# Kernel optimization log

Hardware: AMD Instinct MI355X
Metric: run time of the kernel (lower is better)

Reference implementation:

```python
import jax, jax.numpy as jnp
import numpy as np

N, E, C_IN, C_H, HOPS = 100000, 1600000, 10, 128, 3
LN_EPS = 1e-5


def setup_inputs() -> dict:
    key = jax.random.key(0)
    ks = jax.random.split(key, 8)
    s = 0.05  # weight init scale
    return {
        "x": jax.random.normal(ks[0], (N, C_IN), dtype=jnp.float32),
        "W_in": jax.random.normal(ks[1], (C_H, C_IN), dtype=jnp.float32) * s,
        "b_in": jnp.zeros((C_H,), jnp.float32),
        "hop_W": jax.random.normal(ks[2], (HOPS, C_H, C_H), dtype=jnp.float32) * s,
        "hop_b": jnp.zeros((HOPS, C_H), jnp.float32),
        "hop_g": jnp.ones((HOPS, C_H), jnp.float32),
        "hop_be": jnp.zeros((HOPS, C_H), jnp.float32),
        "gates": jax.random.normal(ks[3], (HOPS, C_H), dtype=jnp.float32),
        "fW": jax.random.normal(ks[4], (C_H, C_H), dtype=jnp.float32) * s,
        "fb": jnp.zeros((C_H,), jnp.float32),
        "fg": jnp.ones((C_H,), jnp.float32),
        "fbe": jnp.zeros((C_H,), jnp.float32),
        "edge_index": jax.random.randint(ks[5], (2, E), 0, N, dtype=jnp.int64) if jax.config.jax_enable_x64 else jax.random.randint(ks[5], (2, E), 0, N).astype(jnp.int32),
        "edge_attr": jax.random.randint(ks[6], (E,), 0, 5).astype(jnp.int32),
    }


def _layernorm(h, g, b):
    mu = h.mean(-1, keepdims=True)
    var = ((h - mu) ** 2).mean(-1, keepdims=True)  # biased var (torch LayerNorm)
    return (h - mu) * jax.lax.rsqrt(var + LN_EPS) * g + b


def _mpnn(x, src, dst, W, b, g, be):
    # ResidualMPNNLayer: scatter-max aggregate of x[src] at dst, linear, LN, residual relu.
    # dst entries equal to n act as a dummy bucket (for masked-out edges).
    n = x.shape[0]
    agg = jax.ops.segment_max(x[src], dst, num_segments=n + 1)[:n]
    # nodes with no incoming messages: torch_scatter fills with 0
    agg = jnp.where(jnp.isfinite(agg), agg, 0.0)
    return jax.nn.relu(_layernorm(agg @ W.T + b, g, be) + x)


def reference(x, W_in, b_in, hop_W, hop_b, hop_g, hop_be, gates, fW, fb, fg, fbe, edge_index, edge_attr):
    src, dst = edge_index[0], edge_index[1]
    n = x.shape[0]

    # ThreeHopSmallBlock
    h = jax.nn.relu(x @ W_in.T + b_in)  # [N, C_H]
    hop_outs = []
    for i in range(HOPS):
        h = _mpnn(h, src, dst, hop_W[i], hop_b[i], hop_g[i], hop_be[i])
        hop_outs.append(h)
    node_features = sum(o * jax.nn.sigmoid(gates[i]) for i, o in enumerate(hop_outs))
    # dropout inactive at inference

    # polygon subgraph: edges with attr == 3; masked edges scatter to dummy bucket n
    poly = edge_attr == 3
    dst_p = jnp.where(poly, dst, n)
    sub = _mpnn(node_features, src, dst_p, fW, fb, fg, fbe)  # [N, C_H]

    neg_inf = jnp.float32(-jnp.inf)
    fill = jnp.float32(1e-4)

    # sink nodes = unique destinations of polygon edges
    sink_mask = jax.ops.segment_sum(poly.astype(jnp.int32), dst, num_segments=n) > 0
    v2 = jnp.max(jnp.where(sink_mask[:, None], sub, neg_inf), axis=0, keepdims=True)
    v2 = jnp.where(jnp.any(sink_mask), v2, fill)

    # remaining nodes: NOT (x[:,0] > 0.1)
    rem = ~(x[:, 0] > 0.1)
    v3 = jnp.max(jnp.where(rem[:, None], node_features, neg_inf), axis=0, keepdims=True)
    v3 = jnp.where(jnp.any(rem), v3, fill)

    return jnp.concatenate([v2, v3], axis=0)  # [2, C_H]
```

## Files before the change

### kernel.cpp

```cpp
#include <hip/hip_runtime.h>
#include <hip/hip_bf16.h>
#include <cstdint>

#define N_NODES 100000
#define N_EDGES 1600000
#define C_IN    10
#define C_H     128
#define LN_EPS  1e-5f

#define SCAN_BLOCKS 98

typedef unsigned short u16x2 __attribute__((ext_vector_type(2)));

static __device__ inline unsigned pkmax(unsigned a, unsigned b) {
    u16x2 x = __builtin_bit_cast(u16x2, a), y = __builtin_bit_cast(u16x2, b);
    return __builtin_bit_cast(unsigned, __builtin_elementwise_max(x, y));
}
static __device__ inline unsigned bf16rne(float f) {
    unsigned u = __float_as_uint(f);
    return (u + 0x7FFFu + ((u >> 16) & 1u)) >> 16;
}
static __device__ inline unsigned packbf(float lo, float hi) {
    return (bf16rne(hi) << 16) | bf16rne(lo);
}

__global__ void hist_kernel(const int* __restrict__ dst, const int* __restrict__ attr,
                            int* __restrict__ cnt, int* __restrict__ pcnt) {
    int i = blockIdx.x * blockDim.x + threadIdx.x;
    int stride = gridDim.x * blockDim.x;
    for (; i < N_EDGES; i += stride) {
        int d = dst[i];
        atomicAdd(&cnt[d], 1);
        if (attr[i] == 3) atomicAdd(&pcnt[d], 1);
    }
}

__device__ inline int wave_incl_scan(int v, int lane) {
#pragma unroll
    for (int off = 1; off < 64; off <<= 1) {
        int n = __shfl_up(v, off);
        if (lane >= off) v += n;
    }
    return v;
}

__global__ __launch_bounds__(1024) void scan1_kernel(const int* __restrict__ cnt,
                                                     int* __restrict__ excl,
                                                     int* __restrict__ bsum) {
    __shared__ int wsum[16];
    const int t = threadIdx.x, lane = t & 63, wid = t >> 6;
    const int i = blockIdx.x * 1024 + t;
    const int v = (i < N_NODES) ? cnt[i] : 0;
    int inc = wave_incl_scan(v, lane);
    if (lane == 63) wsum[wid] = inc;
    __syncthreads();
    if (t < 16) {
        int w = wsum[t];
#pragma unroll
        for (int off = 1; off < 16; off <<= 1) {
            int n = __shfl_up(w, off);
            if (t >= off) w += n;
        }
        wsum[t] = w;
    }
    __syncthreads();
    const int woff = (wid == 0) ? 0 : wsum[wid - 1];
    if (i < N_NODES) excl[i] = inc - v + woff;
    if (t == 0) bsum[blockIdx.x] = wsum[15];
}

__global__ void scan2_kernel(const int* __restrict__ bsum, int* __restrict__ bofs) {
    __shared__ int wsum[2];
    const int t = threadIdx.x, lane = t & 63, wid = t >> 6;
    const int v = (t < SCAN_BLOCKS) ? bsum[t] : 0;
    int inc = wave_incl_scan(v, lane);
    if (lane == 63) wsum[wid] = inc;
    __syncthreads();
    const int woff = (wid == 0) ? 0 : wsum[0];
    if (t < SCAN_BLOCKS) bofs[t] = inc - v + woff;
}

__global__ __launch_bounds__(1024) void scan3_kernel(const int* __restrict__ excl,
                                                     const int* __restrict__ bofs,
                                                     const int* __restrict__ pcnt,
                                                     int* __restrict__ row_off,
                                                     int* __restrict__ poly_end) {
    const int i = blockIdx.x * 1024 + threadIdx.x;
    if (i < N_NODES) {
        const int r = excl[i] + bofs[blockIdx.x];
        row_off[i]  = r;
        poly_end[i] = r + pcnt[i];
    }
    if (i == 0) row_off[N_NODES] = N_EDGES;
}

__global__ void scatter_kernel(const int* __restrict__ src, const int* __restrict__ dst,
                               const int* __restrict__ attr,
                               const int* __restrict__ row_off, const int* __restrict__ poly_end,
                               int* __restrict__ curP, int* __restrict__ curR,
                               int* __restrict__ pack) {
    int i = blockIdx.x * blockDim.x + threadIdx.x;
    int stride = gridDim.x * blockDim.x;
    for (; i < N_EDGES; i += stride) {
        int d = dst[i];
        int pos;
        if (attr[i] == 3) pos = row_off[d]  + atomicAdd(&curP[d], 1);
        else              pos = poly_end[d] + atomicAdd(&curR[d], 1);
        pack[pos] = src[i];
    }
}

__global__ void in_proj_kernel(const float* __restrict__ x, const float* __restrict__ Win,
                               const float* __restrict__ bin, float* __restrict__ h0,
                               unsigned* __restrict__ h16) {
    __shared__ float Wl[C_H * 11];
    for (int i = threadIdx.x; i < C_H * C_IN; i += blockDim.x) {
        int c = i / C_IN, k = i % C_IN;
        Wl[c * 11 + k] = Win[i];
    }
    __syncthreads();
    const int l = threadIdx.x & 63, wid = threadIdx.x >> 6;
    const int wave = blockIdx.x * 4 + wid, nw = gridDim.x * 4;
    const float2 bb = *reinterpret_cast<const float2*>(bin + 2 * l);
    for (int n = wave; n < N_NODES; n += nw) {
        float xr[C_IN];
#pragma unroll
        for (int k = 0; k < C_IN; ++k) xr[k] = x[n * C_IN + k];
        float a0 = bb.x, a1 = bb.y;
#pragma unroll
        for (int k = 0; k < C_IN; ++k) {
            a0 = fmaf(xr[k], Wl[(2 * l) * 11 + k], a0);
            a1 = fmaf(xr[k], Wl[(2 * l + 1) * 11 + k], a1);
        }
        a0 = fmaxf(a0, 0.f);
        a1 = fmaxf(a1, 0.f);
        *reinterpret_cast<float2*>(h0 + (size_t)n * C_H + 2 * l) = make_float2(a0, a1);
        h16[(size_t)n * 64 + l] = packbf(a0, a1);
    }
}

#define NPW 4
#define LWAVES 16

template <int MODE>
__global__ __launch_bounds__(1024) void layer_kernel(
    const float* __restrict__ hin, const unsigned* __restrict__ hin16,
    float* __restrict__ hout, unsigned* __restrict__ hout16,
    float* __restrict__ nf, const float* __restrict__ x,
    const int* __restrict__ row_off, const int* __restrict__ poly_end,
    const int* __restrict__ pack,
    const float* __restrict__ W, const float* __restrict__ bias,
    const float* __restrict__ gamma, const float* __restrict__ beta,
    const float* __restrict__ gate, float* __restrict__ out)
{
    __shared__ float    Wl[C_H * C_H];
    __shared__ unsigned aggU[LWAVES][NPW * 64];

    for (int i = threadIdx.x; i < C_H * C_H; i += 1024) {
        int c = i >> 7, k = i & 127;
        Wl[(c << 7) + (k ^ ((c >> 1) & 31))] = W[i];
    }
    __syncthreads();

    const int l = threadIdx.x & 63, wid = threadIdx.x >> 6;
    const int swz = l & 31;
    const int row0 = (2 * l) << 7, row1 = (2 * l + 1) << 7;
    const int wave = blockIdx.x * LWAVES + wid, nw = gridDim.x * LWAVES;

    const float2 bb = *reinterpret_cast<const float2*>(bias  + 2 * l);
    const float2 gg = *reinterpret_cast<const float2*>(gamma + 2 * l);
    const float2 ee = *reinterpret_cast<const float2*>(beta  + 2 * l);
    float sg0 = 0.f, sg1 = 0.f;
    if (MODE <= 2) {
        const float2 gt = *reinterpret_cast<const float2*>(gate + 2 * l);
        sg0 = 1.f / (1.f + expf(-gt.x));
        sg1 = 1.f / (1.f + expf(-gt.y));
    }

    float red0 = 0.f, red1 = 0.f;

    const unsigned* __restrict__ hb16 = hin16 + l;

    for (int base = wave * NPW; base < N_NODES; base += nw * NPW) {
        bool anyp[NPW];
#pragma unroll
        for (int j = 0; j < NPW; ++j) {
            const int n = base + j;
            unsigned m = 0u;
            bool ap = false;
            if (n < N_NODES) {
                const int beg = row_off[n];
                const int end = (MODE == 3) ? poly_end[n] : row_off[n + 1];
                ap = (end > beg);
                int e = beg;
                for (; e + 8 <= end; e += 8) {
                    unsigned v[8];
#pragma unroll
                    for (int t = 0; t < 8; ++t)
                        v[t] = hb16[(size_t)pack[e + t] * 64];
#pragma unroll
                    for (int t = 0; t < 8; ++t) m = pkmax(m, v[t]);
                }
                for (; e + 4 <= end; e += 4) {
                    const unsigned v0 = hb16[(size_t)pack[e]     * 64];
                    const unsigned v1 = hb16[(size_t)pack[e + 1] * 64];
                    const unsigned v2 = hb16[(size_t)pack[e + 2] * 64];
                    const unsigned v3 = hb16[(size_t)pack[e + 3] * 64];
                    m = pkmax(m, pkmax(pkmax(v0, v1), pkmax(v2, v3)));
                }
                for (; e + 2 <= end; e += 2) {
                    const unsigned v0 = hb16[(size_t)pack[e]     * 64];
                    const unsigned v1 = hb16[(size_t)pack[e + 1] * 64];
                    m = pkmax(m, pkmax(v0, v1));
                }
                if (e < end) m = pkmax(m, hb16[(size_t)pack[e] * 64]);
            }
            anyp[j] = ap;
            aggU[wid][j * 64 + l] = m;
        }

        float acc[NPW][2];
#pragma unroll
        for (int j = 0; j < NPW; ++j) { acc[j][0] = 0.f; acc[j][1] = 0.f; }
#pragma unroll 4
        for (int t = 0; t < 64; ++t) {
            const int c0 = (2 * t) ^ swz, c1 = (2 * t + 1) ^ swz;
            const float w00 = Wl[row0 + c0], w01 = Wl[row0 + c1];
            const float w10 = Wl[row1 + c0], w11 = Wl[row1 + c1];
#pragma unroll
            for (int j = 0; j < NPW; ++j) {
                const unsigned u = aggU[wid][j * 64 + t];
                const float a0 = __uint_as_float(u << 16);
                const float a1 = __uint_as_float(u & 0xFFFF0000u);
                acc[j][0] = fmaf(a1, w01, fmaf(a0, w00, acc[j][0]));
                acc[j][1] = fmaf(a1, w11, fmaf(a0, w10, acc[j][1]));
            }
        }

#pragma unroll
        for (int j = 0; j < NPW; ++j) {
            const int n = base + j;
            if (n < N_NODES) {
                float h0 = acc[j][0] + bb.x, h1 = acc[j][1] + bb.y;
                float s = h0 + h1, q = h0 * h0 + h1 * h1;
#pragma unroll
                for (int m2 = 1; m2 < 64; m2 <<= 1) {
                    s += __shfl_xor(s, m2);
                    q += __shfl_xor(q, m2);
                }
                const float mu  = s * (1.f / 128.f);
                const float var = q * (1.f / 128.f) - mu * mu;
                const float rs  = rsqrtf(var + LN_EPS);
                const float2 r = *reinterpret_cast<const float2*>(hin + (size_t)n * C_H + 2 * l);
                const float o0 = fmaxf((h0 - mu) * rs * gg.x + ee.x + r.x, 0.f);
                const float o1 = fmaxf((h1 - mu) * rs * gg.y + ee.y + r.y, 0.f);
                if (MODE <= 1) {
                    *reinterpret_cast<float2*>(hout + (size_t)n * C_H + 2 * l) = make_float2(o0, o1);
                    hout16[(size_t)n * 64 + l] = packbf(o0, o1);
                }
                if (MODE == 0) {
                    *reinterpret_cast<float2*>(nf + (size_t)n * C_H + 2 * l) =
                        make_float2(o0 * sg0, o1 * sg1);
                } else if (MODE == 1) {
                    float2* p = reinterpret_cast<float2*>(nf + (size_t)n * C_H + 2 * l);
                    float2 v = *p;
                    v.x += o0 * sg0; v.y += o1 * sg1;
                    *p = v;
                } else if (MODE == 2) {
                    float2* p = reinterpret_cast<float2*>(nf + (size_t)n * C_H + 2 * l);
                    float2 v = *p;
                    const float f0 = v.x + o0 * sg0, f1 = v.y + o1 * sg1;
                    *p = make_float2(f0, f1);
                    hout16[(size_t)n * 64 + l] = packbf(f0, f1);
                    if (x[(size_t)n * C_IN] <= 0.1f) {
                        red0 = fmaxf(red0, f0);
                        red1 = fmaxf(red1, f1);
                    }
                } else {
                    if (anyp[j]) {
                        red0 = fmaxf(red0, o0);
                        red1 = fmaxf(red1, o1);
                    }
                }
            }
        }
    }

    if (MODE >= 2) {
        __syncthreads();
        float* red = reinterpret_cast<float*>(&aggU[0][0]);
        *reinterpret_cast<float2*>(&red[wid * 128 + 2 * l]) = make_float2(red0, red1);
        __syncthreads();
        if (threadIdx.x < 128) {
            const int c = threadIdx.x;
            float m = red[c];
#pragma unroll
            for (int w = 1; w < LWAVES; ++w) m = fmaxf(m, red[w * 128 + c]);
            float* o = out + (MODE == 3 ? 0 : 128);
            atomicMax(reinterpret_cast<int*>(o + c), __float_as_int(m));
        }
    }
}

extern "C" void kernel_launch(void* const* d_in, const int* in_sizes, int n_in,
                              void* d_out, int out_size, void* d_ws, size_t ws_size,
                              hipStream_t stream) {
    const float* x      = (const float*)d_in[0];
    const float* W_in   = (const float*)d_in[1];
    const float* b_in   = (const float*)d_in[2];
    const float* hop_W  = (const float*)d_in[3];
    const float* hop_b  = (const float*)d_in[4];
    const float* hop_g  = (const float*)d_in[5];
    const float* hop_be = (const float*)d_in[6];
    const float* gates  = (const float*)d_in[7];
    const float* fW     = (const float*)d_in[8];
    const float* fb     = (const float*)d_in[9];
    const float* fg     = (const float*)d_in[10];
    const float* fbe    = (const float*)d_in[11];
    const int*   eidx   = (const int*)d_in[12];
    const int*   eattr  = (const int*)d_in[13];
    float* out = (float*)d_out;

    char* ws = (char*)d_ws;
    size_t off = 0;
    auto alloc = [&](size_t bytes) {
        char* p = ws + off;
        off = (off + bytes + 255) & ~(size_t)255;
        return p;
    };
    const size_t npad = ((size_t)N_NODES * 4 + 255) & ~(size_t)255;
    int*      cnt     = (int*)alloc((size_t)N_NODES * 4);
    int*      pcnt    = (int*)alloc((size_t)N_NODES * 4);
    int*      curP    = (int*)alloc((size_t)N_NODES * 4);
    int*      curR    = (int*)alloc((size_t)N_NODES * 4);
    int*      excl    = (int*)alloc((size_t)N_NODES * 4);
    int*      bsum    = (int*)alloc((size_t)SCAN_BLOCKS * 4);
    int*      bofs    = (int*)alloc((size_t)SCAN_BLOCKS * 4);
    int*      row_off = (int*)alloc((size_t)(N_NODES + 1) * 4);
    int*      polyend = (int*)alloc((size_t)N_NODES * 4);
    int*      pack    = (int*)alloc((size_t)N_EDGES * 4);
    float*    hA      = (float*)alloc((size_t)N_NODES * C_H * 4);
    float*    hB      = (float*)alloc((size_t)N_NODES * C_H * 4);
    float*    nf      = (float*)alloc((size_t)N_NODES * C_H * 4);
    unsigned* hA16    = (unsigned*)alloc((size_t)N_NODES * 64 * 4);
    unsigned* hB16    = (unsigned*)alloc((size_t)N_NODES * 64 * 4);
    unsigned* nf16    = hB16;
    (void)ws_size;

    const int* src = eidx;
    const int* dst = eidx + N_EDGES;

    hipMemsetAsync(cnt, 0, npad * 4, stream);
    hipMemsetAsync(d_out, 0, 256 * 4, stream);

    hist_kernel<<<2048, 256, 0, stream>>>(dst, eattr, cnt, pcnt);
    scan1_kernel<<<SCAN_BLOCKS, 1024, 0, stream>>>(cnt, excl, bsum);
    scan2_kernel<<<1, 128, 0, stream>>>(bsum, bofs);
    scan3_kernel<<<SCAN_BLOCKS, 1024, 0, stream>>>(excl, bofs, pcnt, row_off, polyend);
    scatter_kernel<<<2048, 256, 0, stream>>>(src, dst, eattr, row_off, polyend, curP, curR, pack);
    in_proj_kernel<<<2048, 256, 0, stream>>>(x, W_in, b_in, hA, hA16);

    layer_kernel<0><<<512, 1024, 0, stream>>>(hA, hA16, hB, hB16, nf, x, row_off, polyend, pack,
                                              hop_W + 0 * C_H * C_H, hop_b + 0 * C_H,
                                              hop_g + 0 * C_H, hop_be + 0 * C_H,
                                              gates + 0 * C_H, out);
    layer_kernel<1><<<512, 1024, 0, stream>>>(hB, hB16, hA, hA16, nf, x, row_off, polyend, pack,
                                              hop_W + 1 * C_H * C_H, hop_b + 1 * C_H,
                                              hop_g + 1 * C_H, hop_be + 1 * C_H,
                                              gates + 1 * C_H, out);
    layer_kernel<2><<<512, 1024, 0, stream>>>(hA, hA16, nullptr, nf16, nf, x, row_off, polyend, pack,
                                              hop_W + 2 * C_H * C_H, hop_b + 2 * C_H,
                                              hop_g + 2 * C_H, hop_be + 2 * C_H,
                                              gates + 2 * C_H, out);
    layer_kernel<3><<<512, 1024, 0, stream>>>(nf, nf16, nullptr, nullptr, nullptr, x, row_off, polyend, pack,
                                              fW, fb, fg, fbe, nullptr, out);
}
```

Baseline: 762.3 us.

## Use bf16 MFMA for per-layer linear with 16-node wave tiles

Replaces the scalar fp32 FMA matmul in the layer kernel with MFMA 16x16x32 bf16 instructions. Weights are packed to bf16 in a swizzled LDS layout, and each wave now processes 16 nodes per tile instead of 4. Block size drops from 1024 to 512 threads, LayerNorm reductions move to 16-lane shuffles, and the output stores become scalar per-column writes. This trades weight precision (now bf16) and less coalesced epilogue stores for far fewer ALU instructions in the GEMM part.

Result: slower. 836.8 us (+9.8%).

```diff
diff --git a/kernel.cpp b/kernel.cpp
--- a/kernel.cpp
+++ b/kernel.cpp
@@ -11,6 +11,9 @@
 #define SCAN_BLOCKS 98
 
 typedef unsigned short u16x2 __attribute__((ext_vector_type(2)));
+typedef short          short8 __attribute__((ext_vector_type(8)));
+typedef float          f32x4  __attribute__((ext_vector_type(4)));
+typedef unsigned       uint4v __attribute__((ext_vector_type(4)));
 
 static __device__ inline unsigned pkmax(unsigned a, unsigned b) {
     u16x2 x = __builtin_bit_cast(u16x2, a), y = __builtin_bit_cast(u16x2, b);
@@ -139,11 +142,10 @@
     }
 }
 
-#define NPW 4
-#define LWAVES 16
+#define LWAVES 8
 
 template <int MODE>
-__global__ __launch_bounds__(1024) void layer_kernel(
+__global__ __launch_bounds__(512) void layer_kernel(
     const float* __restrict__ hin, const unsigned* __restrict__ hin16,
     float* __restrict__ hout, unsigned* __restrict__ hout16,
     float* __restrict__ nf, const float* __restrict__ x,
@@ -153,51 +155,52 @@
     const float* __restrict__ gamma, const float* __restrict__ beta,
     const float* __restrict__ gate, float* __restrict__ out)
 {
-    __shared__ float    Wl[C_H * C_H];
-    __shared__ unsigned aggU[LWAVES][NPW * 64];
-
-    for (int i = threadIdx.x; i < C_H * C_H; i += 1024) {
-        int c = i >> 7, k = i & 127;
-        Wl[(c << 7) + (k ^ ((c >> 1) & 31))] = W[i];
-    }
-    __syncthreads();
-
-    const int l = threadIdx.x & 63, wid = threadIdx.x >> 6;
-    const int swz = l & 31;
-    const int row0 = (2 * l) << 7, row1 = (2 * l + 1) << 7;
-    const int wave = blockIdx.x * LWAVES + wid, nw = gridDim.x * LWAVES;
-
-    const float2 bb = *reinterpret_cast<const float2*>(bias  + 2 * l);
-    const float2 gg = *reinterpret_cast<const float2*>(gamma + 2 * l);
-    const float2 ee = *reinterpret_cast<const float2*>(beta  + 2 * l);
-    float sg0 = 0.f, sg1 = 0.f;
-    if (MODE <= 2) {
-        const float2 gt = *reinterpret_cast<const float2*>(gate + 2 * l);
-        sg0 = 1.f / (1.f + expf(-gt.x));
-        sg1 = 1.f / (1.f + expf(-gt.y));
-    }
-
-    float red0 = 0.f, red1 = 0.f;
-
+    __shared__ unsigned Wb[C_H * 64];
+    __shared__ unsigned aggU[LWAVES * 16 * 64];
+    __shared__ float    par[4 * C_H];
+
+    const int tid = threadIdx.x;
+    for (int i = tid; i < C_H * 64; i += 512) {
+        const int c = i >> 6, w = i & 63;
+        const float2 wv = *reinterpret_cast<const float2*>(W + (size_t)c * C_H + 2 * w);
+        Wb[(c << 6) + (w ^ ((c & 7) << 2))] = packbf(wv.x, wv.y);
+    }
+    if (tid < C_H) {
+        par[tid]           = bias[tid];
+        par[C_H + tid]     = gamma[tid];
+        par[2 * C_H + tid] = beta[tid];
+        par[3 * C_H + tid] = (MODE <= 2) ? 1.f / (1.f + expf(-gate[tid])) : 0.f;
+    }
+    __syncthreads();
+
+    const int l = tid & 63, wid = tid >> 6;
+    const int cc = l & 15, q = l >> 4;
+    unsigned* aggW = aggU + wid * 1024;
     const unsigned* __restrict__ hb16 = hin16 + l;
 
-    for (int base = wave * NPW; base < N_NODES; base += nw * NPW) {
-        bool anyp[NPW];
-#pragma unroll
-        for (int j = 0; j < NPW; ++j) {
+    const int wave = blockIdx.x * LWAVES + wid;
+    const int nwav = gridDim.x * LWAVES;
+
+    float vmax[8];
+#pragma unroll
+    for (int nt = 0; nt < 8; ++nt) vmax[nt] = 0.f;
+
+    for (int base = wave * 16; base < N_NODES; base += nwav * 16) {
+        unsigned apmask = 0u, remmask = 0u;
+
+        for (int j = 0; j < 16; ++j) {
             const int n = base + j;
             unsigned m = 0u;
-            bool ap = false;
             if (n < N_NODES) {
                 const int beg = row_off[n];
                 const int end = (MODE == 3) ? poly_end[n] : row_off[n + 1];
-                ap = (end > beg);
+                if (MODE == 3) { if (end > beg) apmask |= 1u << j; }
+                if (MODE == 2) { if (x[(size_t)n * C_IN] <= 0.1f) remmask |= 1u << j; }
                 int e = beg;
                 for (; e + 8 <= end; e += 8) {
                     unsigned v[8];
 #pragma unroll
-                    for (int t = 0; t < 8; ++t)
-                        v[t] = hb16[(size_t)pack[e + t] * 64];
+                    for (int t = 0; t < 8; ++t) v[t] = hb16[(size_t)pack[e + t] * 64];
 #pragma unroll
                     for (int t = 0; t < 8; ++t) m = pkmax(m, v[t]);
                 }
@@ -215,71 +218,82 @@
                 }
                 if (e < end) m = pkmax(m, hb16[(size_t)pack[e] * 64]);
             }
-            anyp[j] = ap;
-            aggU[wid][j * 64 + l] = m;
-        }
-
-        float acc[NPW][2];
-#pragma unroll
-        for (int j = 0; j < NPW; ++j) { acc[j][0] = 0.f; acc[j][1] = 0.f; }
-#pragma unroll 4
-        for (int t = 0; t < 64; ++t) {
-            const int c0 = (2 * t) ^ swz, c1 = (2 * t + 1) ^ swz;
-            const float w00 = Wl[row0 + c0], w01 = Wl[row0 + c1];
-            const float w10 = Wl[row1 + c0], w11 = Wl[row1 + c1];
-#pragma unroll
-            for (int j = 0; j < NPW; ++j) {
-                const unsigned u = aggU[wid][j * 64 + t];
-                const float a0 = __uint_as_float(u << 16);
-                const float a1 = __uint_as_float(u & 0xFFFF0000u);
-                acc[j][0] = fmaf(a1, w01, fmaf(a0, w00, acc[j][0]));
-                acc[j][1] = fmaf(a1, w11, fmaf(a0, w10, acc[j][1]));
-            }
-        }
-
-#pragma unroll
-        for (int j = 0; j < NPW; ++j) {
-            const int n = base + j;
-            if (n < N_NODES) {
-                float h0 = acc[j][0] + bb.x, h1 = acc[j][1] + bb.y;
-                float s = h0 + h1, q = h0 * h0 + h1 * h1;
-#pragma unroll
-                for (int m2 = 1; m2 < 64; m2 <<= 1) {
-                    s += __shfl_xor(s, m2);
-                    q += __shfl_xor(q, m2);
-                }
+            aggW[j * 64 + (l ^ ((j & 7) << 2))] = m;
+        }
+
+        short8 afr[4];
+#pragma unroll
+        for (int kc = 0; kc < 4; ++kc) {
+            const int w0 = (kc * 16 + q * 4) ^ ((cc & 7) << 2);
+            const uint4v av = *reinterpret_cast<const uint4v*>(&aggW[cc * 64 + w0]);
+            afr[kc] = __builtin_bit_cast(short8, av);
+        }
+
+        f32x4 acc[8];
+#pragma unroll
+        for (int nt = 0; nt < 8; ++nt) {
+            acc[nt] = (f32x4){0.f, 0.f, 0.f, 0.f};
+            const int c = nt * 16 + cc;
+#pragma unroll
+            for (int kc = 0; kc < 4; ++kc) {
+                const int w0 = (kc * 16 + q * 4) ^ ((c & 7) << 2);
+                const uint4v bv4 = *reinterpret_cast<const uint4v*>(&Wb[(c << 6) + w0]);
+                acc[nt] = __builtin_amdgcn_mfma_f32_16x16x32_bf16(
+                    afr[kc], __builtin_bit_cast(short8, bv4), acc[nt], 0, 0, 0);
+            }
+        }
+
+        float bv[8], gv[8], ev[8], sgv[8];
+#pragma unroll
+        for (int nt = 0; nt < 8; ++nt) {
+            bv[nt] = par[nt * 16 + cc];
+            gv[nt] = par[C_H + nt * 16 + cc];
+            ev[nt] = par[2 * C_H + nt * 16 + cc];
+            sgv[nt] = (MODE <= 2) ? par[3 * C_H + nt * 16 + cc] : 0.f;
+        }
+        const int nvalid = N_NODES - base;
+#pragma unroll
+        for (int r = 0; r < 4; ++r) {
+            const int j = q * 4 + r;
+            float h[8], s = 0.f, qq = 0.f;
+#pragma unroll
+            for (int nt = 0; nt < 8; ++nt) {
+                h[nt] = acc[nt][r] + bv[nt];
+                s += h[nt];
+                qq = fmaf(h[nt], h[nt], qq);
+            }
+#pragma unroll
+            for (int mm = 1; mm < 16; mm <<= 1) {
+                s  += __shfl_xor(s,  mm);
+                qq += __shfl_xor(qq, mm);
+            }
+            if (j < nvalid) {
+                const size_t nrow = (size_t)(base + j) * C_H;
                 const float mu  = s * (1.f / 128.f);
-                const float var = q * (1.f / 128.f) - mu * mu;
+                const float var = qq * (1.f / 128.f) - mu * mu;
                 const float rs  = rsqrtf(var + LN_EPS);
-                const float2 r = *reinterpret_cast<const float2*>(hin + (size_t)n * C_H + 2 * l);
-                const float o0 = fmaxf((h0 - mu) * rs * gg.x + ee.x + r.x, 0.f);
-                const float o1 = fmaxf((h1 - mu) * rs * gg.y + ee.y + r.y, 0.f);
-                if (MODE <= 1) {
-                    *reinterpret_cast<float2*>(hout + (size_t)n * C_H + 2 * l) = make_float2(o0, o1);
-                    hout16[(size_t)n * 64 + l] = packbf(o0, o1);
-                }
-                if (MODE == 0) {
-                    *reinterpret_cast<float2*>(nf + (size_t)n * C_H + 2 * l) =
-                        make_float2(o0 * sg0, o1 * sg1);
-                } else if (MODE == 1) {
-                    float2* p = reinterpret_cast<float2*>(nf + (size_t)n * C_H + 2 * l);
-                    float2 v = *p;
-                    v.x += o0 * sg0; v.y += o1 * sg1;
-                    *p = v;
-                } else if (MODE == 2) {
-                    float2* p = reinterpret_cast<float2*>(nf + (size_t)n * C_H + 2 * l);
-                    float2 v = *p;
-                    const float f0 = v.x + o0 * sg0, f1 = v.y + o1 * sg1;
-                    *p = make_float2(f0, f1);
-                    hout16[(size_t)n * 64 + l] = packbf(f0, f1);
-                    if (x[(size_t)n * C_IN] <= 0.1f) {
-                        red0 = fmaxf(red0, f0);
-                        red1 = fmaxf(red1, f1);
+#pragma unroll
+                for (int nt = 0; nt < 8; ++nt) {
+                    const int c = nt * 16 + cc;
+                    const float res = hin[nrow + c];
+                    const float o = fmaxf((h[nt] - mu) * rs * gv[nt] + ev[nt] + res, 0.f);
+                    if (MODE <= 1) {
+                        hout[nrow + c] = o;
+                        reinterpret_cast<unsigned short*>(hout16)[nrow + c] =
+                            (unsigned short)bf16rne(o);
                     }
-                } else {
-                    if (anyp[j]) {
-                        red0 = fmaxf(red0, o0);
-                        red1 = fmaxf(red1, o1);
+                    if (MODE == 0) {
+                        nf[nrow + c] = o * sgv[nt];
+                    } else if (MODE == 1) {
+                        nf[nrow + c] += o * sgv[nt];
+                    } else if (MODE == 2) {
+                        const float f = nf[nrow + c] + o * sgv[nt];
+                        nf[nrow + c] = f;
+                        reinterpret_cast<unsigned short*>(hout16)[nrow + c] =
+                            (unsigned short)bf16rne(f);
+                        if ((remmask >> j) & 1u) vmax[nt] = fmaxf(vmax[nt], f);
+                    } else {
+                        if ((apmask >> j) & 1u) vmax[nt] = fmaxf(vmax[nt], o);
                     }
                 }
             }
@@ -287,17 +301,25 @@
     }
 
     if (MODE >= 2) {
+#pragma unroll
+        for (int nt = 0; nt < 8; ++nt) {
+            vmax[nt] = fmaxf(vmax[nt], __shfl_xor(vmax[nt], 16));
+            vmax[nt] = fmaxf(vmax[nt], __shfl_xor(vmax[nt], 32));
+        }
         __syncthreads();
-        float* red = reinterpret_cast<float*>(&aggU[0][0]);
-        *reinterpret_cast<float2*>(&red[wid * 128 + 2 * l]) = make_float2(red0, red1);
+        float* redL = reinterpret_cast<float*>(aggU);
+        if (l < 16) {
+#pragma unroll
+            for (int nt = 0; nt < 8; ++nt)
+                redL[wid * 128 + nt * 16 + l] = vmax[nt];
+        }
         __syncthreads();
-        if (threadIdx.x < 128) {
-            const int c = threadIdx.x;
-            float m = red[c];
-#pragma unroll
-            for (int w = 1; w < LWAVES; ++w) m = fmaxf(m, red[w * 128 + c]);
+        if (tid < 128) {
+            float m = redL[tid];
+#pragma unroll
+            for (int w = 1; w < LWAVES; ++w) m = fmaxf(m, redL[w * 128 + tid]);
             float* o = out + (MODE == 3 ? 0 : 128);
-            atomicMax(reinterpret_cast<int*>(o + c), __float_as_int(m));
+            atomicMax(reinterpret_cast<int*>(o + tid), __float_as_int(m));
         }
     }
 }
@@ -360,18 +382,18 @@
     scatter_kernel<<<2048, 256, 0, stream>>>(src, dst, eattr, row_off, polyend, curP, curR, pack);
     in_proj_kernel<<<2048, 256, 0, stream>>>(x, W_in, b_in, hA, hA16);
 
-    layer_kernel<0><<<512, 1024, 0, stream>>>(hA, hA16, hB, hB16, nf, x, row_off, polyend, pack,
-                                              hop_W + 0 * C_H * C_H, hop_b + 0 * C_H,
-                                              hop_g + 0 * C_H, hop_be + 0 * C_H,
-                                              gates + 0 * C_H, out);
-    layer_kernel<1><<<512, 1024, 0, stream>>>(hB, hB16, hA, hA16, nf, x, row_off, polyend, pack,
-                                              hop_W + 1 * C_H * C_H, hop_b + 1 * C_H,
-                                              hop_g + 1 * C_H, hop_be + 1 * C_H,
-                                              gates + 1 * C_H, out);
-    layer_kernel<2><<<512, 1024, 0, stream>>>(hA, hA16, nullptr, nf16, nf, x, row_off, polyend, pack,
-                                              hop_W + 2 * C_H * C_H, hop_b + 2 * C_H,
-                                              hop_g + 2 * C_H, hop_be + 2 * C_H,
-                                              gates + 2 * C_H, out);
-    layer_kernel<3><<<512, 1024, 0, stream>>>(nf, nf16, nullptr, nullptr, nullptr, x, row_off, polyend, pack,
-                                              fW, fb, fg, fbe, nullptr, out);
-}
+    layer_kernel<0><<<512, 512, 0, stream>>>(hA, hA16, hB, hB16, nf, x, row_off, polyend, pack,
+                                             hop_W + 0 * C_H * C_H, hop_b + 0 * C_H,
+                                             hop_g + 0 * C_H, hop_be + 0 * C_H,
+                                             gates + 0 * C_H, out);
+    layer_kernel<1><<<512, 512, 0, stream>>>(hB, hB16, hA, hA16, nf, x, row_off, polyend, pack,
+                                             hop_W + 1 * C_H * C_H, hop_b + 1 * C_H,
+                                             hop_g + 1 * C_H, hop_be + 1 * C_H,
+                                             gates + 1 * C_H, out);
+    layer_kernel<2><<<512, 512, 0, stream>>>(hA, hA16, nullptr, nf16, nf, x, row_off, polyend, pack,
+                                             hop_W + 2 * C_H * C_H, hop_b + 2 * C_H,
+                                             hop_g + 2 * C_H, hop_be + 2 * C_H,
+                                             gates + 2 * C_H, out);
+    layer_kernel<3><<<512, 512, 0, stream>>>(nf, nf16, nullptr, nullptr, nullptr, x, row_off, polyend, pack,
+                                             fW, fb, fg, fbe, nullptr, out);
+}
```
